# Kernel tuning notes

Hardware: AMD Instinct MI355X
Metric: run time of the kernel (lower is better)

Reference implementation:

```python
import jax, jax.numpy as jnp
import numpy as np

D_MODEL = 256
NUM_TYPES = 20
T_MAX = 200.0
LENGTH_SCALE = 1.0
ALPHA = 1.0
LN_EPS = 1e-6


def setup_inputs() -> dict:
    key = jax.random.key(0)
    kt, ktype, kat, kw, kwt, kbt = jax.random.split(key, 6)
    B, S = 4, 4096
    # event times: sorted uniform in [0, T_MAX] per sequence
    event_time = jnp.sort(jax.random.uniform(kt, (B, S), jnp.float32) * T_MAX, axis=-1)
    event_type = jax.random.randint(ktype, (B, S), 1, NUM_TYPES + 1, jnp.int32)
    arrival_times = jax.random.uniform(kat, (B, S), jnp.float32) * T_MAX
    # decoder params: input_weights (no bias), event_time_calculator (d->1, bias)
    W_in = jax.random.normal(kw, (D_MODEL, D_MODEL), jnp.float32) / np.sqrt(D_MODEL)
    w_t = jax.random.normal(kwt, (D_MODEL,), jnp.float32) / np.sqrt(D_MODEL)
    b_t = jax.random.normal(kbt, (), jnp.float32)
    ln_gamma = jnp.ones((D_MODEL,), jnp.float32)
    ln_beta = jnp.zeros((D_MODEL,), jnp.float32)
    return {"event_type": event_type, "event_time": event_time,
            "arrival_times": arrival_times, "W_in": W_in, "w_t": w_t,
            "b_t": b_t, "ln_gamma": ln_gamma, "ln_beta": ln_beta}


def reference(event_type, event_time, arrival_times, W_in, w_t, b_t, ln_gamma, ln_beta):
    B, S = event_time.shape
    # sinusoidal temporal encoding: w_k[i] = 10000^(2*(i//2+1)/d_model)
    i = jnp.arange(D_MODEL)
    w_k = jnp.power(10000.0, 2.0 * (i // 2 + 1).astype(jnp.float32) / D_MODEL)
    te = event_time[:, :, None] / w_k                       # [B,S,D]
    embedding = jnp.where(i % 2 == 0, jnp.sin(te), jnp.cos(te))
    # squared-exponential kernel on pairwise time differences, causal-masked
    dt = event_time[:, :, None] - event_time[:, None, :]    # [B,S,S]
    scores = ALPHA * jnp.exp(-(dt * dt) / (2.0 * LENGTH_SCALE ** 2))
    causal = jnp.tril(jnp.ones((S, S), bool))               # keep j <= i
    scores = jnp.where(causal, scores, 0.0)
    hidden = jnp.einsum('bij,bjd->bid', scores, embedding)  # [B,S,D]
    # LayerNorm (eps=1e-6)
    mu = hidden.mean(-1, keepdims=True)
    var = jnp.mean((hidden - mu) ** 2, axis=-1, keepdims=True)
    hidden = (hidden - mu) * jax.lax.rsqrt(var + LN_EPS) * ln_gamma + ln_beta
    # decoder: relu(linear) -> softplus(linear->1)
    hs = jax.nn.relu(jnp.einsum('bsd,ed->bse', hidden, W_in))
    out = jax.nn.softplus(jnp.einsum('bsd,d->bs', hs, w_t) + b_t)
    return out
```

## Files before the change

### kernel.cpp

```cpp
#include <hip/hip_runtime.h>
#include <hip/hip_bf16.h>
#include <math.h>

#define D 256
#define S 4096
#define BATCH 4
#define RPB 16
#define NBLK (BATCH * S / RPB)
#define DT_CUT 7.0f

typedef __attribute__((ext_vector_type(8))) short short8;
typedef __attribute__((ext_vector_type(4))) float f32x4;

static __device__ __forceinline__ unsigned short f2bf(float x) {
    union { __hip_bfloat16 b; unsigned short u; } cv;
    cv.b = __float2bfloat16(x);
    return cv.u;
}


__global__ __launch_bounds__(256) void embt_kernel(const float* __restrict__ t,
                                                   const float* __restrict__ W,
                                                   unsigned short* __restrict__ emb5,
                                                   unsigned short* __restrict__ w5,
                                                   int* __restrict__ jcmin_out) {
    int blk = blockIdx.x;
    int tid = threadIdx.x;

    if (blk < 256) {
        int e = blk, dd = tid;
        int wv = e >> 6, et = (e >> 4) & 3, l15 = e & 15;
        int kt = dd >> 5, kgg = (dd >> 3) & 3, ee = dd & 7;
        w5[(size_t)(((wv * 4 + et) * 8 + kt) * 512) + (kgg * 16 + l15) * 8 + ee]
            = f2bf(W[e * D + dd]);
    }

    if (tid < 64) {
#pragma unroll
        for (int s = 0; s < 2; ++s) {
            int fb = blk * 2 + s;
            int b2 = fb >> 8;
            int i0 = (fb & 255) * RPB;
            const float* tb2 = t + b2 * S;
            float tcut = tb2[i0] - DT_CUT;
            int lo = 0, hi = i0;
            while (hi > lo) {
                int step = ((hi - lo) + 63) >> 6;
                int p = min(lo + tid * step, hi);
                unsigned long long mb = __ballot(tb2[p] < tcut);
                int cnt = __popcll(mb);
                int nlo = (cnt == 0) ? lo : (lo + (cnt - 1) * step + 1);
                int nhi = (cnt == 0) ? nlo : min(lo + cnt * step, hi);
                lo = nlo; hi = nhi;
            }
            if (tid == 0) jcmin_out[fb] = lo >> 5;
        }
    }

    __shared__ unsigned short tile[8192];
    int j_local = tid & 31;
    int fg      = tid >> 5;
    int b       = blk >> 7;
    int jc      = blk & 127;
    float tv = t[b * S + jc * 32 + j_local];
    int kg = j_local >> 3, e = j_local & 7;
    const float c2 = -0.1038102552f;
#pragma unroll
    for (int kk = 0; kk < 16; ++kk) {
        int k = fg * 16 + kk;
        float te = tv * exp2f(c2 * (float)(k + 1));
        float sn, cs;
        __sincosf(te, &sn, &cs);
        int base = (k >> 3) * 512 + kg * 128 + e;
        int ln0 = 2 * (k & 7);
        tile[base + ln0 * 8]       = f2bf(sn);
        tile[base + (ln0 + 1) * 8] = f2bf(cs);
    }
    __syncthreads();
    const uint4* src = (const uint4*)tile;
    uint4* dst = (uint4*)(emb5 + (size_t)blk * 8192);
#pragma unroll
    for (int p = 0; p < 4; ++p) dst[p * 256 + tid] = src[p * 256 + tid];
}

__global__ __launch_bounds__(256, 4) void fused_kernel(
    const float* __restrict__ t, const unsigned short* __restrict__ emb5,
    const unsigned short* __restrict__ w5, const int* __restrict__ jcmin_arr,
    const float* __restrict__ gamma, const float* __restrict__ beta,
    const float* __restrict__ w_t, const float* __restrict__ b_t,
    float* __restrict__ out) {
    int bid  = blockIdx.x;
    int blk  = (bid & 7) * (NBLK / 8) + (bid >> 3);
    int b    = blk >> 8;
    int i0   = (blk & 255) * RPB;
    int tid  = threadIdx.x;
    int w    = tid >> 6;
    int lane = tid & 63;
    int ln15 = lane & 15;
    int kg   = lane >> 4;
    const float* tb = t + b * S;

    float ti = tb[i0 + ln15];
    int irow = i0 + ln15;
    int jcmin = jcmin_arr[blk];
    int jcmax = (i0 + RPB - 1) >> 5;

    f32x4 acc[4];
#pragma unroll
    for (int nt = 0; nt < 4; ++nt) acc[nt] = (f32x4){0.f, 0.f, 0.f, 0.f};

    const unsigned short* ebase =
        emb5 + ((size_t)(b * 128) * 16 + w * 4) * 512 + lane * 8;
    short8 c0, c1, c2, c3;
    float4 ta, tb4;
    {
        const unsigned short* p = ebase + (size_t)jcmin * 8192;
        c0 = *(const short8*)(p);
        c1 = *(const short8*)(p + 512);
        c2 = *(const short8*)(p + 1024);
        c3 = *(const short8*)(p + 1536);
        ta  = *(const float4*)&tb[jcmin * 32 + kg * 8];
        tb4 = *(const float4*)&tb[jcmin * 32 + kg * 8 + 4];
    }
    for (int jc = jcmin; jc <= jcmax; ++jc) {
        int j0 = jc * 32;
        short8 n0, n1, n2, n3;
        float4 nta, ntb;
        if (jc < jcmax) {
            const unsigned short* p = ebase + (size_t)(jc + 1) * 8192;
            n0 = *(const short8*)(p);
            n1 = *(const short8*)(p + 512);
            n2 = *(const short8*)(p + 1024);
            n3 = *(const short8*)(p + 1536);
            nta = *(const float4*)&tb[j0 + 32 + kg * 8];
            ntb = *(const float4*)&tb[j0 + 32 + kg * 8 + 4];
        }
        float tj[8] = {ta.x, ta.y, ta.z, ta.w, tb4.x, tb4.y, tb4.z, tb4.w};
        union { short8 v; unsigned short u[8]; } a;
        if (j0 + 31 <= i0) {
#pragma unroll
            for (int e = 0; e < 8; ++e) {
                float dt = ti - tj[e];
                a.u[e] = f2bf(__expf(-0.5f * dt * dt));
            }
        } else {
#pragma unroll
            for (int e = 0; e < 8; ++e) {
                float dt = ti - tj[e];
                float sc = __expf(-0.5f * dt * dt);
                a.u[e] = (j0 + kg * 8 + e <= irow) ? f2bf(sc) : (unsigned short)0;
            }
        }
        acc[0] = __builtin_amdgcn_mfma_f32_16x16x32_bf16(a.v, c0, acc[0], 0, 0, 0);
        acc[1] = __builtin_amdgcn_mfma_f32_16x16x32_bf16(a.v, c1, acc[1], 0, 0, 0);
        acc[2] = __builtin_amdgcn_mfma_f32_16x16x32_bf16(a.v, c2, acc[2], 0, 0, 0);
        acc[3] = __builtin_amdgcn_mfma_f32_16x16x32_bf16(a.v, c3, acc[3], 0, 0, 0);
        c0 = n0; c1 = n1; c2 = n2; c3 = n3;
        ta = nta; tb4 = ntb;
    }

    const unsigned short* wbase = w5 + (size_t)(w * 4 * 8) * 512 + lane * 8;
    short8 w0 = *(const short8*)(wbase + (size_t)(0 * 8) * 512);
    short8 w1 = *(const short8*)(wbase + (size_t)(1 * 8) * 512);
    short8 w2 = *(const short8*)(wbase + (size_t)(2 * 8) * 512);
    short8 w3 = *(const short8*)(wbase + (size_t)(3 * 8) * 512);

    __shared__ float2 s_ln[4][RPB];
    __shared__ unsigned short H[RPB][264];
    __shared__ float s_dec[4][RPB];

#pragma unroll
    for (int reg = 0; reg < 4; ++reg) {
        float s = acc[0][reg] + acc[1][reg] + acc[2][reg] + acc[3][reg];
        float q = acc[0][reg] * acc[0][reg] + acc[1][reg] * acc[1][reg]
                + acc[2][reg] * acc[2][reg] + acc[3][reg] * acc[3][reg];
#pragma unroll
        for (int m = 1; m < 16; m <<= 1) {
            s += __shfl_xor(s, m);
            q += __shfl_xor(q, m);
        }
        if (ln15 == 0) s_ln[w][kg * 4 + reg] = make_float2(s, q);
    }
    __syncthreads();

    float g[4], be[4];
#pragma unroll
    for (int nt = 0; nt < 4; ++nt) {
        g[nt]  = gamma[w * 64 + nt * 16 + ln15];
        be[nt] = beta[w * 64 + nt * 16 + ln15];
    }
#pragma unroll
    for (int reg = 0; reg < 4; ++reg) {
        int r = kg * 4 + reg;
        float2 p0 = s_ln[0][r], p1 = s_ln[1][r], p2 = s_ln[2][r], p3 = s_ln[3][r];
        float sum = p0.x + p1.x + p2.x + p3.x;
        float sq  = p0.y + p1.y + p2.y + p3.y;
        float mu  = sum * (1.0f / D);
        float var = fmaxf(sq * (1.0f / D) - mu * mu, 0.0f);
        float rstd = rsqrtf(var + 1e-6f);
#pragma unroll
        for (int nt = 0; nt < 4; ++nt) {
            float h = (acc[nt][reg] - mu) * rstd * g[nt] + be[nt];
            H[r][w * 64 + nt * 16 + ln15] = f2bf(h);
        }
    }
    __syncthreads();

    f32x4 acc2[4];
#pragma unroll
    for (int et = 0; et < 4; ++et) acc2[et] = (f32x4){0.f, 0.f, 0.f, 0.f};

    short8 afr[8];
#pragma unroll
    for (int kt = 0; kt < 8; ++kt)
        afr[kt] = *(const short8*)&H[ln15][kt * 32 + kg * 8];

#pragma unroll
    for (int kt = 0; kt < 8; ++kt) {
        short8 nw0, nw1, nw2, nw3;
        if (kt < 7) {
            const unsigned short* p = wbase + (size_t)(kt + 1) * 512;
            nw0 = *(const short8*)(p + (size_t)(0 * 8) * 512);
            nw1 = *(const short8*)(p + (size_t)(1 * 8) * 512);
            nw2 = *(const short8*)(p + (size_t)(2 * 8) * 512);
            nw3 = *(const short8*)(p + (size_t)(3 * 8) * 512);
        }
        acc2[0] = __builtin_amdgcn_mfma_f32_16x16x32_bf16(afr[kt], w0, acc2[0], 0, 0, 0);
        acc2[1] = __builtin_amdgcn_mfma_f32_16x16x32_bf16(afr[kt], w1, acc2[1], 0, 0, 0);
        acc2[2] = __builtin_amdgcn_mfma_f32_16x16x32_bf16(afr[kt], w2, acc2[2], 0, 0, 0);
        acc2[3] = __builtin_amdgcn_mfma_f32_16x16x32_bf16(afr[kt], w3, acc2[3], 0, 0, 0);
        w0 = nw0; w1 = nw1; w2 = nw2; w3 = nw3;
    }

    float wt[4];
#pragma unroll
    for (int et = 0; et < 4; ++et) wt[et] = w_t[w * 64 + et * 16 + ln15];
#pragma unroll
    for (int reg = 0; reg < 4; ++reg) {
        float v = 0.f;
#pragma unroll
        for (int et = 0; et < 4; ++et)
            v = fmaf(fmaxf(acc2[et][reg], 0.f), wt[et], v);
#pragma unroll
        for (int m = 1; m < 16; m <<= 1) v += __shfl_xor(v, m);
        if (ln15 == 0) s_dec[w][kg * 4 + reg] = v;
    }
    __syncthreads();
    if (tid < RPB) {
        float tot = s_dec[0][tid] + s_dec[1][tid] + s_dec[2][tid] + s_dec[3][tid] + b_t[0];
        float o = fmaxf(tot, 0.0f) + log1pf(expf(-fabsf(tot)));
        out[(size_t)blk * RPB + tid] = o;
    }
}

extern "C" void kernel_launch(void* const* d_in, const int* in_sizes, int n_in,
                              void* d_out, int out_size, void* d_ws, size_t ws_size,
                              hipStream_t stream) {
    const float* t   = (const float*)d_in[1];
    const float* W   = (const float*)d_in[3];
    const float* wt  = (const float*)d_in[4];
    const float* bt  = (const float*)d_in[5];
    const float* gam = (const float*)d_in[6];
    const float* bet = (const float*)d_in[7];
    float* out = (float*)d_out;

    char* ws = (char*)d_ws;
    unsigned short* emb5  = (unsigned short*)ws;
    unsigned short* w5    = (unsigned short*)(ws + (size_t)8388608);
    int*            jcmin = (int*)(ws + (size_t)8519680);

    embt_kernel<<<dim3(512), dim3(256), 0, stream>>>(t, W, emb5, w5, jcmin);
    fused_kernel<<<dim3(NBLK), dim3(256), 0, stream>>>(
        t, emb5, w5, jcmin, gam, bet, wt, bt, out);
}
```

Before: 25.59 us.

## Split decoder into separate kernel and double rows per band block

```diff
diff --git a/kernel.cpp b/kernel.cpp
--- a/kernel.cpp
+++ b/kernel.cpp
@@ -5,7 +5,7 @@
 #define D 256
 #define S 4096
 #define BATCH 4
-#define RPB 16
+#define RPB 32
 #define NBLK (BATCH * S / RPB)
 #define DT_CUT 7.0f
 
@@ -29,32 +29,28 @@
 
     if (blk < 256) {
         int e = blk, dd = tid;
-        int wv = e >> 6, et = (e >> 4) & 3, l15 = e & 15;
+        int et16 = e >> 4, l15 = e & 15;
         int kt = dd >> 5, kgg = (dd >> 3) & 3, ee = dd & 7;
-        w5[(size_t)(((wv * 4 + et) * 8 + kt) * 512) + (kgg * 16 + l15) * 8 + ee]
+        w5[(size_t)((et16 * 8 + kt) * 512) + (kgg * 16 + l15) * 8 + ee]
             = f2bf(W[e * D + dd]);
     }
 
     if (tid < 64) {
-#pragma unroll
-        for (int s = 0; s < 2; ++s) {
-            int fb = blk * 2 + s;
-            int b2 = fb >> 8;
-            int i0 = (fb & 255) * RPB;
-            const float* tb2 = t + b2 * S;
-            float tcut = tb2[i0] - DT_CUT;
-            int lo = 0, hi = i0;
-            while (hi > lo) {
-                int step = ((hi - lo) + 63) >> 6;
-                int p = min(lo + tid * step, hi);
-                unsigned long long mb = __ballot(tb2[p] < tcut);
-                int cnt = __popcll(mb);
-                int nlo = (cnt == 0) ? lo : (lo + (cnt - 1) * step + 1);
-                int nhi = (cnt == 0) ? nlo : min(lo + cnt * step, hi);
-                lo = nlo; hi = nhi;
-            }
-            if (tid == 0) jcmin_out[fb] = lo >> 5;
-        }
+        int b2 = blk >> 7;
+        int i0 = (blk & 127) * RPB;
+        const float* tb2 = t + b2 * S;
+        float tcut = tb2[i0] - DT_CUT;
+        int lo = 0, hi = i0;
+        while (hi > lo) {
+            int step = ((hi - lo) + 63) >> 6;
+            int p = min(lo + tid * step, hi);
+            unsigned long long mb = __ballot(tb2[p] < tcut);
+            int cnt = __popcll(mb);
+            int nlo = (cnt == 0) ? lo : (lo + (cnt - 1) * step + 1);
+            int nhi = (cnt == 0) ? nlo : min(lo + cnt * step, hi);
+            lo = nlo; hi = nhi;
+        }
+        if (tid == 0) jcmin_out[blk] = lo >> 5;
     }
 
     __shared__ unsigned short tile[8192];
@@ -83,16 +79,15 @@
     for (int p = 0; p < 4; ++p) dst[p * 256 + tid] = src[p * 256 + tid];
 }
 
-__global__ __launch_bounds__(256, 4) void fused_kernel(
+__global__ __launch_bounds__(256, 4) void band_kernel(
     const float* __restrict__ t, const unsigned short* __restrict__ emb5,
-    const unsigned short* __restrict__ w5, const int* __restrict__ jcmin_arr,
+    const int* __restrict__ jcmin_arr,
     const float* __restrict__ gamma, const float* __restrict__ beta,
-    const float* __restrict__ w_t, const float* __restrict__ b_t,
-    float* __restrict__ out) {
+    unsigned short* __restrict__ H5) {
     int bid  = blockIdx.x;
     int blk  = (bid & 7) * (NBLK / 8) + (bid >> 3);
-    int b    = blk >> 8;
-    int i0   = (blk & 255) * RPB;
+    int b    = blk >> 7;
+    int i0   = (blk & 127) * RPB;
     int tid  = threadIdx.x;
     int w    = tid >> 6;
     int lane = tid & 63;
@@ -100,87 +95,96 @@
     int kg   = lane >> 4;
     const float* tb = t + b * S;
 
-    float ti = tb[i0 + ln15];
-    int irow = i0 + ln15;
+    float ti0 = tb[i0 + ln15], ti1 = tb[i0 + 16 + ln15];
+    int   ir0 = i0 + ln15,     ir1 = i0 + 16 + ln15;
     int jcmin = jcmin_arr[blk];
-    int jcmax = (i0 + RPB - 1) >> 5;
-
-    f32x4 acc[4];
-#pragma unroll
-    for (int nt = 0; nt < 4; ++nt) acc[nt] = (f32x4){0.f, 0.f, 0.f, 0.f};
+    int jcmax = i0 >> 5;
+
+    f32x4 acc[2][4];
+#pragma unroll
+    for (int Mt = 0; Mt < 2; ++Mt)
+#pragma unroll
+        for (int nt = 0; nt < 4; ++nt) acc[Mt][nt] = (f32x4){0.f, 0.f, 0.f, 0.f};
 
     const unsigned short* ebase =
         emb5 + ((size_t)(b * 128) * 16 + w * 4) * 512 + lane * 8;
     short8 c0, c1, c2, c3;
-    float4 ta, tb4;
+    float4 ta4, tb4;
     {
         const unsigned short* p = ebase + (size_t)jcmin * 8192;
         c0 = *(const short8*)(p);
         c1 = *(const short8*)(p + 512);
         c2 = *(const short8*)(p + 1024);
         c3 = *(const short8*)(p + 1536);
-        ta  = *(const float4*)&tb[jcmin * 32 + kg * 8];
+        ta4 = *(const float4*)&tb[jcmin * 32 + kg * 8];
         tb4 = *(const float4*)&tb[jcmin * 32 + kg * 8 + 4];
     }
-    for (int jc = jcmin; jc <= jcmax; ++jc) {
-        int j0 = jc * 32;
-        short8 n0, n1, n2, n3;
-        float4 nta, ntb;
-        if (jc < jcmax) {
-            const unsigned short* p = ebase + (size_t)(jc + 1) * 8192;
-            n0 = *(const short8*)(p);
-            n1 = *(const short8*)(p + 512);
-            n2 = *(const short8*)(p + 1024);
-            n3 = *(const short8*)(p + 1536);
-            nta = *(const float4*)&tb[j0 + 32 + kg * 8];
-            ntb = *(const float4*)&tb[j0 + 32 + kg * 8 + 4];
-        }
-        float tj[8] = {ta.x, ta.y, ta.z, ta.w, tb4.x, tb4.y, tb4.z, tb4.w};
-        union { short8 v; unsigned short u[8]; } a;
-        if (j0 + 31 <= i0) {
-#pragma unroll
-            for (int e = 0; e < 8; ++e) {
-                float dt = ti - tj[e];
-                a.u[e] = f2bf(__expf(-0.5f * dt * dt));
-            }
-        } else {
-#pragma unroll
-            for (int e = 0; e < 8; ++e) {
-                float dt = ti - tj[e];
-                float sc = __expf(-0.5f * dt * dt);
-                a.u[e] = (j0 + kg * 8 + e <= irow) ? f2bf(sc) : (unsigned short)0;
-            }
-        }
-        acc[0] = __builtin_amdgcn_mfma_f32_16x16x32_bf16(a.v, c0, acc[0], 0, 0, 0);
-        acc[1] = __builtin_amdgcn_mfma_f32_16x16x32_bf16(a.v, c1, acc[1], 0, 0, 0);
-        acc[2] = __builtin_amdgcn_mfma_f32_16x16x32_bf16(a.v, c2, acc[2], 0, 0, 0);
-        acc[3] = __builtin_amdgcn_mfma_f32_16x16x32_bf16(a.v, c3, acc[3], 0, 0, 0);
+    for (int jc = jcmin; jc < jcmax; ++jc) {
+        const unsigned short* p = ebase + (size_t)(jc + 1) * 8192;
+        short8 n0 = *(const short8*)(p);
+        short8 n1 = *(const short8*)(p + 512);
+        short8 n2 = *(const short8*)(p + 1024);
+        short8 n3 = *(const short8*)(p + 1536);
+        float4 nta = *(const float4*)&tb[jc * 32 + 32 + kg * 8];
+        float4 ntb = *(const float4*)&tb[jc * 32 + 32 + kg * 8 + 4];
+
+        float tj[8] = {ta4.x, ta4.y, ta4.z, ta4.w, tb4.x, tb4.y, tb4.z, tb4.w};
+        union { short8 v; unsigned short u[8]; } a0, a1;
+#pragma unroll
+        for (int e = 0; e < 8; ++e) {
+            float d0 = ti0 - tj[e], d1 = ti1 - tj[e];
+            a0.u[e] = f2bf(__expf(-0.5f * d0 * d0));
+            a1.u[e] = f2bf(__expf(-0.5f * d1 * d1));
+        }
+        acc[0][0] = __builtin_amdgcn_mfma_f32_16x16x32_bf16(a0.v, c0, acc[0][0], 0, 0, 0);
+        acc[0][1] = __builtin_amdgcn_mfma_f32_16x16x32_bf16(a0.v, c1, acc[0][1], 0, 0, 0);
+        acc[0][2] = __builtin_amdgcn_mfma_f32_16x16x32_bf16(a0.v, c2, acc[0][2], 0, 0, 0);
+        acc[0][3] = __builtin_amdgcn_mfma_f32_16x16x32_bf16(a0.v, c3, acc[0][3], 0, 0, 0);
+        acc[1][0] = __builtin_amdgcn_mfma_f32_16x16x32_bf16(a1.v, c0, acc[1][0], 0, 0, 0);
+        acc[1][1] = __builtin_amdgcn_mfma_f32_16x16x32_bf16(a1.v, c1, acc[1][1], 0, 0, 0);
+        acc[1][2] = __builtin_amdgcn_mfma_f32_16x16x32_bf16(a1.v, c2, acc[1][2], 0, 0, 0);
+        acc[1][3] = __builtin_amdgcn_mfma_f32_16x16x32_bf16(a1.v, c3, acc[1][3], 0, 0, 0);
         c0 = n0; c1 = n1; c2 = n2; c3 = n3;
-        ta = nta; tb4 = ntb;
-    }
-
-    const unsigned short* wbase = w5 + (size_t)(w * 4 * 8) * 512 + lane * 8;
-    short8 w0 = *(const short8*)(wbase + (size_t)(0 * 8) * 512);
-    short8 w1 = *(const short8*)(wbase + (size_t)(1 * 8) * 512);
-    short8 w2 = *(const short8*)(wbase + (size_t)(2 * 8) * 512);
-    short8 w3 = *(const short8*)(wbase + (size_t)(3 * 8) * 512);
+        ta4 = nta; tb4 = ntb;
+    }
+    {
+        int j0 = jcmax * 32;
+        float tj[8] = {ta4.x, ta4.y, ta4.z, ta4.w, tb4.x, tb4.y, tb4.z, tb4.w};
+        union { short8 v; unsigned short u[8]; } a0, a1;
+#pragma unroll
+        for (int e = 0; e < 8; ++e) {
+            int j = j0 + kg * 8 + e;
+            float d0 = ti0 - tj[e], d1 = ti1 - tj[e];
+            float s0 = __expf(-0.5f * d0 * d0), s1 = __expf(-0.5f * d1 * d1);
+            a0.u[e] = (j <= ir0) ? f2bf(s0) : (unsigned short)0;
+            a1.u[e] = (j <= ir1) ? f2bf(s1) : (unsigned short)0;
+        }
+        acc[0][0] = __builtin_amdgcn_mfma_f32_16x16x32_bf16(a0.v, c0, acc[0][0], 0, 0, 0);
+        acc[0][1] = __builtin_amdgcn_mfma_f32_16x16x32_bf16(a0.v, c1, acc[0][1], 0, 0, 0);
+        acc[0][2] = __builtin_amdgcn_mfma_f32_16x16x32_bf16(a0.v, c2, acc[0][2], 0, 0, 0);
+        acc[0][3] = __builtin_amdgcn_mfma_f32_16x16x32_bf16(a0.v, c3, acc[0][3], 0, 0, 0);
+        acc[1][0] = __builtin_amdgcn_mfma_f32_16x16x32_bf16(a1.v, c0, acc[1][0], 0, 0, 0);
+        acc[1][1] = __builtin_amdgcn_mfma_f32_16x16x32_bf16(a1.v, c1, acc[1][1], 0, 0, 0);
+        acc[1][2] = __builtin_amdgcn_mfma_f32_16x16x32_bf16(a1.v, c2, acc[1][2], 0, 0, 0);
+        acc[1][3] = __builtin_amdgcn_mfma_f32_16x16x32_bf16(a1.v, c3, acc[1][3], 0, 0, 0);
+    }
 
     __shared__ float2 s_ln[4][RPB];
     __shared__ unsigned short H[RPB][264];
-    __shared__ float s_dec[4][RPB];
-
-#pragma unroll
-    for (int reg = 0; reg < 4; ++reg) {
-        float s = acc[0][reg] + acc[1][reg] + acc[2][reg] + acc[3][reg];
-        float q = acc[0][reg] * acc[0][reg] + acc[1][reg] * acc[1][reg]
-                + acc[2][reg] * acc[2][reg] + acc[3][reg] * acc[3][reg];
-#pragma unroll
-        for (int m = 1; m < 16; m <<= 1) {
-            s += __shfl_xor(s, m);
-            q += __shfl_xor(q, m);
-        }
-        if (ln15 == 0) s_ln[w][kg * 4 + reg] = make_float2(s, q);
-    }
+#pragma unroll
+    for (int Mt = 0; Mt < 2; ++Mt)
+#pragma unroll
+        for (int reg = 0; reg < 4; ++reg) {
+            float s = acc[Mt][0][reg] + acc[Mt][1][reg] + acc[Mt][2][reg] + acc[Mt][3][reg];
+            float q = acc[Mt][0][reg] * acc[Mt][0][reg] + acc[Mt][1][reg] * acc[Mt][1][reg]
+                    + acc[Mt][2][reg] * acc[Mt][2][reg] + acc[Mt][3][reg] * acc[Mt][3][reg];
+#pragma unroll
+            for (int m = 1; m < 16; m <<= 1) {
+                s += __shfl_xor(s, m);
+                q += __shfl_xor(q, m);
+            }
+            if (ln15 == 0) s_ln[w][Mt * 16 + kg * 4 + reg] = make_float2(s, q);
+        }
     __syncthreads();
 
     float g[4], be[4];
@@ -190,66 +194,95 @@
         be[nt] = beta[w * 64 + nt * 16 + ln15];
     }
 #pragma unroll
-    for (int reg = 0; reg < 4; ++reg) {
-        int r = kg * 4 + reg;
-        float2 p0 = s_ln[0][r], p1 = s_ln[1][r], p2 = s_ln[2][r], p3 = s_ln[3][r];
-        float sum = p0.x + p1.x + p2.x + p3.x;
-        float sq  = p0.y + p1.y + p2.y + p3.y;
-        float mu  = sum * (1.0f / D);
-        float var = fmaxf(sq * (1.0f / D) - mu * mu, 0.0f);
-        float rstd = rsqrtf(var + 1e-6f);
-#pragma unroll
-        for (int nt = 0; nt < 4; ++nt) {
-            float h = (acc[nt][reg] - mu) * rstd * g[nt] + be[nt];
-            H[r][w * 64 + nt * 16 + ln15] = f2bf(h);
-        }
-    }
-    __syncthreads();
-
-    f32x4 acc2[4];
-#pragma unroll
-    for (int et = 0; et < 4; ++et) acc2[et] = (f32x4){0.f, 0.f, 0.f, 0.f};
-
-    short8 afr[8];
-#pragma unroll
-    for (int kt = 0; kt < 8; ++kt)
-        afr[kt] = *(const short8*)&H[ln15][kt * 32 + kg * 8];
-
-#pragma unroll
-    for (int kt = 0; kt < 8; ++kt) {
-        short8 nw0, nw1, nw2, nw3;
-        if (kt < 7) {
-            const unsigned short* p = wbase + (size_t)(kt + 1) * 512;
-            nw0 = *(const short8*)(p + (size_t)(0 * 8) * 512);
-            nw1 = *(const short8*)(p + (size_t)(1 * 8) * 512);
-            nw2 = *(const short8*)(p + (size_t)(2 * 8) * 512);
-            nw3 = *(const short8*)(p + (size_t)(3 * 8) * 512);
-        }
-        acc2[0] = __builtin_amdgcn_mfma_f32_16x16x32_bf16(afr[kt], w0, acc2[0], 0, 0, 0);
-        acc2[1] = __builtin_amdgcn_mfma_f32_16x16x32_bf16(afr[kt], w1, acc2[1], 0, 0, 0);
-        acc2[2] = __builtin_amdgcn_mfma_f32_16x16x32_bf16(afr[kt], w2, acc2[2], 0, 0, 0);
-        acc2[3] = __builtin_amdgcn_mfma_f32_16x16x32_bf16(afr[kt], w3, acc2[3], 0, 0, 0);
-        w0 = nw0; w1 = nw1; w2 = nw2; w3 = nw3;
-    }
-
-    float wt[4];
-#pragma unroll
-    for (int et = 0; et < 4; ++et) wt[et] = w_t[w * 64 + et * 16 + ln15];
-#pragma unroll
-    for (int reg = 0; reg < 4; ++reg) {
-        float v = 0.f;
-#pragma unroll
-        for (int et = 0; et < 4; ++et)
-            v = fmaf(fmaxf(acc2[et][reg], 0.f), wt[et], v);
-#pragma unroll
-        for (int m = 1; m < 16; m <<= 1) v += __shfl_xor(v, m);
-        if (ln15 == 0) s_dec[w][kg * 4 + reg] = v;
-    }
-    __syncthreads();
-    if (tid < RPB) {
-        float tot = s_dec[0][tid] + s_dec[1][tid] + s_dec[2][tid] + s_dec[3][tid] + b_t[0];
+    for (int Mt = 0; Mt < 2; ++Mt)
+#pragma unroll
+        for (int reg = 0; reg < 4; ++reg) {
+            int r = Mt * 16 + kg * 4 + reg;
+            float2 p0 = s_ln[0][r], p1 = s_ln[1][r], p2 = s_ln[2][r], p3 = s_ln[3][r];
+            float sum = p0.x + p1.x + p2.x + p3.x;
+            float sq  = p0.y + p1.y + p2.y + p3.y;
+            float mu  = sum * (1.0f / D);
+            float var = fmaxf(sq * (1.0f / D) - mu * mu, 0.0f);
+            float rstd = rsqrtf(var + 1e-6f);
+#pragma unroll
+            for (int nt = 0; nt < 4; ++nt) {
+                float h = (acc[Mt][nt][reg] - mu) * rstd * g[nt] + be[nt];
+                H[r][w * 64 + nt * 16 + ln15] = f2bf(h);
+            }
+        }
+    __syncthreads();
+
+#pragma unroll
+    for (int p = 0; p < 4; ++p) {
+        int f = p * 256 + tid;
+        int tl = f >> 6;
+        int l2 = f & 63;
+        int rb = tl >> 3, kt = tl & 7;
+        int kg2 = l2 >> 4, l15 = l2 & 15;
+        uint4 v = *(const uint4*)&H[rb * 16 + l15][kt * 32 + kg2 * 8];
+        *(uint4*)(H5 + (size_t)blk * 8192 + (size_t)f * 8) = v;
+    }
+}
+
+__global__ __launch_bounds__(512) void decoder_kernel(
+    const unsigned short* __restrict__ H5, const unsigned short* __restrict__ w5,
+    const float* __restrict__ w_t, const float* __restrict__ b_t,
+    float* __restrict__ out) {
+    int blkD = blockIdx.x;
+    int tid  = threadIdx.x;
+    int w    = tid >> 6;
+    int lane = tid & 63;
+    int ln15 = lane & 15;
+    int kg   = lane >> 4;
+
+    __shared__ unsigned short Ald[16384];
+    __shared__ float s_part[8][64];
+
+    const uint4* src = (const uint4*)(H5 + (size_t)blkD * 16384);
+#pragma unroll
+    for (int p = 0; p < 4; ++p) ((uint4*)Ald)[p * 512 + tid] = src[p * 512 + tid];
+
+    short8 wfr[2][8];
+#pragma unroll
+    for (int etL = 0; etL < 2; ++etL)
+#pragma unroll
+        for (int kt = 0; kt < 8; ++kt)
+            wfr[etL][kt] = *(const short8*)(
+                w5 + (size_t)(((2 * w + etL) * 8 + kt) * 512) + lane * 8);
+
+    float wt2[2];
+    wt2[0] = w_t[w * 32 + ln15];
+    wt2[1] = w_t[w * 32 + 16 + ln15];
+    __syncthreads();
+
+#pragma unroll
+    for (int rg = 0; rg < 4; ++rg) {
+        short8 af[8];
+#pragma unroll
+        for (int kt = 0; kt < 8; ++kt)
+            af[kt] = *(const short8*)&Ald[(rg * 8 + kt) * 512 + lane * 8];
+        f32x4 a0 = (f32x4){0.f, 0.f, 0.f, 0.f};
+        f32x4 a1 = (f32x4){0.f, 0.f, 0.f, 0.f};
+#pragma unroll
+        for (int kt = 0; kt < 8; ++kt) {
+            a0 = __builtin_amdgcn_mfma_f32_16x16x32_bf16(af[kt], wfr[0][kt], a0, 0, 0, 0);
+            a1 = __builtin_amdgcn_mfma_f32_16x16x32_bf16(af[kt], wfr[1][kt], a1, 0, 0, 0);
+        }
+#pragma unroll
+        for (int reg = 0; reg < 4; ++reg) {
+            float v = fmaf(fmaxf(a0[reg], 0.f), wt2[0], fmaxf(a1[reg], 0.f) * wt2[1]);
+#pragma unroll
+            for (int m = 1; m < 16; m <<= 1) v += __shfl_xor(v, m);
+            if (ln15 == 0) s_part[w][rg * 16 + kg * 4 + reg] = v;
+        }
+    }
+    __syncthreads();
+    if (tid < 64) {
+        float tot = b_t[0];
+#pragma unroll
+        for (int ww = 0; ww < 8; ++ww) tot += s_part[ww][tid];
         float o = fmaxf(tot, 0.0f) + log1pf(expf(-fabsf(tot)));
-        out[(size_t)blk * RPB + tid] = o;
+        out[(size_t)blkD * 64 + tid] = o;
     }
 }
 
@@ -268,8 +301,9 @@
     unsigned short* emb5  = (unsigned short*)ws;
     unsigned short* w5    = (unsigned short*)(ws + (size_t)8388608);
     int*            jcmin = (int*)(ws + (size_t)8519680);
+    unsigned short* H5    = (unsigned short*)(ws + (size_t)8527872);
 
     embt_kernel<<<dim3(512), dim3(256), 0, stream>>>(t, W, emb5, w5, jcmin);
-    fused_kernel<<<dim3(NBLK), dim3(256), 0, stream>>>(
-        t, emb5, w5, jcmin, gam, bet, wt, bt, out);
-}
+    band_kernel<<<dim3(NBLK), dim3(256), 0, stream>>>(t, emb5, jcmin, gam, bet, H5);
+    decoder_kernel<<<dim3(256), dim3(512), 0, stream>>>(H5, w5, wt, bt, out);
+}
```

Measured after the change: 32.39 us. +26.6%, slower.
